# Performance work log

Hardware: AMD Instinct MI355X
Metric: run time of the kernel (lower is better)

Reference implementation:

```python
import jax, jax.numpy as jnp
import numpy as np

NUM_HEADS = 12
ROPE_THETA = 100.0

def _rotate_half(x):
    x1 = x[..., ::2]
    x2 = x[..., 1::2]
    return jnp.stack((-x2, x1), axis=-1).reshape(x.shape)

def _apply_rope(x, cos, sin):
    return x * cos + _rotate_half(x) * sin

def _rope_cos_sin(h, w, head_dim, theta):
    quarter = head_dim // 4  # head_dim=64 -> 16 freq bands
    inv_freq = 1.0 / theta ** (jnp.arange(quarter, dtype=jnp.float32) / max(quarter, 1))
    y = jnp.repeat(jnp.arange(h, dtype=jnp.float32), w)   # [h*w]
    xc = jnp.tile(jnp.arange(w, dtype=jnp.float32), h)    # [h*w]
    y_freqs = y[:, None] * inv_freq[None, :]               # [N, quarter]
    x_freqs = xc[:, None] * inv_freq[None, :]
    y_ang = jnp.repeat(y_freqs, 2, axis=-1)                # [N, half]
    x_ang = jnp.repeat(x_freqs, 2, axis=-1)
    ang = jnp.concatenate([y_ang, x_ang], axis=-1)         # [N, head_dim]
    return jnp.cos(ang)[None, None], jnp.sin(ang)[None, None]  # [1,1,N,hd]

def setup_inputs() -> dict:
    key = jax.random.key(0)
    ks = jax.random.split(key, 8)
    B, S, D = 8, 1025, 768
    s = 0.02
    return {
        "x": jax.random.normal(ks[0], (B, S, D), jnp.float32),
        "q_w": jax.random.normal(ks[1], (D, D), jnp.float32) * s,
        "q_b": jax.random.normal(ks[2], (D,), jnp.float32) * s,
        "k_w": jax.random.normal(ks[3], (D, D), jnp.float32) * s,
        "v_w": jax.random.normal(ks[4], (D, D), jnp.float32) * s,
        "v_b": jax.random.normal(ks[5], (D,), jnp.float32) * s,
        "o_w": jax.random.normal(ks[6], (D, D), jnp.float32) * s,
        "o_b": jax.random.normal(ks[7], (D,), jnp.float32) * s,
        "h": 32,
        "w": 32,
        "num_prefix_tokens": 1,
    }

def reference(x, q_w, q_b, k_w, v_w, v_b, o_w, o_b, h, w, num_prefix_tokens):
    B, S, D = x.shape
    H = NUM_HEADS
    hd = D // H
    scale = hd ** -0.5
    p = num_prefix_tokens

    def proj(W, b):
        y = jnp.einsum('bsd,ed->bse', x, W)
        if b is not None:
            y = y + b
        return y.reshape(B, S, H, hd).transpose(0, 2, 1, 3)  # [B,H,S,hd]

    q = proj(q_w, q_b)
    k = proj(k_w, None)
    v = proj(v_w, v_b)

    cos, sin = _rope_cos_sin(h, w, hd, ROPE_THETA)
    q = jnp.concatenate([q[:, :, :p], _apply_rope(q[:, :, p:], cos, sin)], axis=2)
    k = jnp.concatenate([k[:, :, :p], _apply_rope(k[:, :, p:], cos, sin)], axis=2)

    attn = jnp.einsum('bhqd,bhkd->bhqk', q * scale, k)
    attn = jax.nn.softmax(attn, axis=-1)
    out = jnp.einsum('bhqk,bhkd->bhqd', attn, v)
    out = out.transpose(0, 2, 1, 3).reshape(B, S, D)
    return jnp.einsum('bsd,ed->bse', out, o_w) + o_b
```

## Files before the change

kernel.cpp:

```cpp
#include <hip/hip_runtime.h>

typedef unsigned short u16;
typedef unsigned int   u32;
typedef __attribute__((ext_vector_type(4))) short s4;
typedef __attribute__((ext_vector_type(8))) short s8;
typedef __attribute__((ext_vector_type(4))) float f4;
typedef __attribute__((ext_vector_type(16))) float f16v;

#define NB   8
#define SEQ  1025
#define DIM  768
#define NH   12
#define HD   64
#define MV   8200
#define SQP  1040
#define SKP  1088
#define NG16 68
#define NQKV 2304
#define BHT  96
#define QSCALE 0.1803368801111204f

__device__ __forceinline__ u16 f2bf(float f) {
  u32 u = __builtin_bit_cast(u32, f);
  u += 0x7fffu + ((u >> 16) & 1u);
  return (u16)(u >> 16);
}
__device__ __forceinline__ float bf2f(u16 h) {
  return __builtin_bit_cast(float, ((u32)h) << 16);
}
__device__ __forceinline__ float exp2f_(float x) {
#if __has_builtin(__builtin_amdgcn_exp2f)
  return __builtin_amdgcn_exp2f(x);
#else
  return exp2f(x);
#endif
}
__device__ __forceinline__ u32 cvtpk(float a, float b) {
  u32 r;
  asm("v_cvt_pk_bf16_f32 %0, %1, %2" : "=v"(r) : "v"(a), "v"(b));
  return r;
}

typedef const __attribute__((address_space(1))) void cas1v;
typedef __attribute__((address_space(3))) void as3v;
__device__ __forceinline__ void gload16(const void* g, void* l) {
  __builtin_amdgcn_global_load_lds((cas1v*)g, (as3v*)l, 16, 0, 0);
}

#define MFMA16(a, b, c) __builtin_amdgcn_mfma_f32_16x16x32_bf16(a, b, c, 0, 0, 0)
#define MFMA32(a, b, c) __builtin_amdgcn_mfma_f32_32x32x16_bf16(a, b, c, 0, 0, 0)

__global__ void conv_x(const float* __restrict__ x, u16* __restrict__ xb) {
  int i = blockIdx.x * 256 + threadIdx.x;
  int e = i * 4;
  int row = e / DIM;
  s4 o;
  if (row < MV) {
    float4 v = *(const float4*)(x + e);
    o[0] = (short)f2bf(v.x); o[1] = (short)f2bf(v.y);
    o[2] = (short)f2bf(v.z); o[3] = (short)f2bf(v.w);
  } else {
    o = (s4){0, 0, 0, 0};
  }
  *(s4*)(xb + e) = o;
}

__global__ void conv_w(const float* __restrict__ qw, const float* __restrict__ kw,
                       const float* __restrict__ vw, const float* __restrict__ ow,
                       const float* __restrict__ qb, const float* __restrict__ vb,
                       u16* __restrict__ wqkv, u16* __restrict__ wo, float* __restrict__ biasq) {
  int i = blockIdx.x * 256 + threadIdx.x;
  wqkv[i]           = f2bf(qw[i]);
  wqkv[i + 589824]  = f2bf(kw[i]);
  wqkv[i + 1179648] = f2bf(vw[i]);
  wo[i]             = f2bf(ow[i]);
  if (i < NQKV) biasq[i] = (i < 768) ? qb[i] : (i < 1536 ? 0.f : vb[i - 1536]);
}

template <int MODE>
__global__ __launch_bounds__(256) void gemm_bt(const u16* __restrict__ A, const u16* __restrict__ Bm,
                                               float* __restrict__ Cf, const float* __restrict__ bias,
                                               u16* __restrict__ Ql, u16* __restrict__ Kl,
                                               u16* __restrict__ Vp,
                                               int N, int K, int Mvalid, int nnt) {
  __shared__ u16 As[2][128 * 32];
  __shared__ u16 Bs[2][128 * 32];
  int tid = threadIdx.x;
  int lane = tid & 63, wave = tid >> 6;
  int g = lane >> 4, c16 = lane & 15;
  int nwg = gridDim.x, orig = blockIdx.x;
  int qd = nwg >> 3, rm = nwg & 7, xcd = orig & 7;
  int wgid = (xcd < rm ? xcd * (qd + 1) : rm * (qd + 1) + (xcd - rm) * qd) + (orig >> 3);
  int m0 = (wgid / nnt) * 128, n0 = (wgid % nnt) * 128;
  int wm = wave >> 1, wn = wave & 1;
  f4 acc[4][4] = {};

  int ldrow = wave * 16 + (lane >> 2);
  int ldk = (lane & 3) * 8;
  const u16* Asrc = A + (size_t)(m0 + ldrow) * K + ldk;
  const u16* Bsrc = Bm + (size_t)(n0 + ldrow) * K + ldk;

  auto stage = [&](int buf, int k0) {
    u16* aw = &As[buf][wave * 512];
    u16* bw = &Bs[buf][wave * 512];
    gload16(Asrc + k0, aw);
    gload16(Asrc + 64 * K + k0, aw + 2048);
    gload16(Bsrc + k0, bw);
    gload16(Bsrc + 64 * K + k0, bw + 2048);
  };

  stage(0, 0);
  __syncthreads();
  int nk = K >> 5;
  for (int t = 0; t < nk; t++) {
    int buf = t & 1;
    if (t + 1 < nk) stage(buf ^ 1, (t + 1) << 5);
    s8 af[4], bf[4];
#pragma unroll
    for (int i = 0; i < 4; i++) {
      af[i] = *(const s8*)(&As[buf][(wm * 64 + i * 16 + c16) * 32 + g * 8]);
      bf[i] = *(const s8*)(&Bs[buf][(wn * 64 + i * 16 + c16) * 32 + g * 8]);
    }
    __builtin_amdgcn_s_setprio(1);
#pragma unroll
    for (int i = 0; i < 4; i++)
#pragma unroll
      for (int j = 0; j < 4; j++)
        acc[i][j] = MFMA16(af[i], bf[j], acc[i][j]);
    __builtin_amdgcn_s_setprio(0);
    __syncthreads();
  }

#pragma unroll
  for (int i = 0; i < 4; i++)
#pragma unroll
    for (int j = 0; j < 4; j++) {
      int n = n0 + wn * 64 + j * 16 + c16;
      float bv = bias[n];
#pragma unroll
      for (int r = 0; r < 4; r++) {
        int m = m0 + wm * 64 + i * 16 + g * 4 + r;
        if (m < Mvalid) {
          float v = acc[i][j][r] + bv;
          if (MODE == 1) {
            Cf[(size_t)m * N + n] = v;
          } else {
            int b = m / 1025, s = m - b * 1025;
            int nh6 = n >> 6, part = nh6 / 12, hq = nh6 - part * 12, d = n & 63;
            u16 o = f2bf(v);
            if (part == 0)      Ql[((size_t)((b * NH + hq) * SQP + s)) * HD + d] = o;
            else if (part == 1) Kl[((size_t)((b * NH + hq) * SKP + s)) * HD + d] = o;
            else {
              int g16 = s >> 4, rr = s & 15;
              int mp = (rr & 3) | (((rr >> 3) & 1) << 2) | (((rr >> 2) & 1) << 3);
              Vp[((size_t)((b * NH + hq) * NG16 + g16) * HD + d) * 16 + mp] = o;
            }
          }
        }
      }
    }
}

__global__ void rope_qk(u16* __restrict__ Ql, u16* __restrict__ Kl) {
  int t = blockIdx.x * 256 + threadIdx.x;
  int j = t & 31;
  int rem = t >> 5;
  int s = rem % SKP;
  int bh = rem / SKP;
  if (bh >= BHT) return;
  size_t qoff = ((size_t)(bh * SQP + s)) * HD + 2 * j;
  size_t koff = ((size_t)(bh * SKP + s)) * HD + 2 * j;
  if (s >= SEQ) {
    *(u32*)(Kl + koff) = 0;
    if (s < SQP) *(u32*)(Ql + qoff) = 0;
    return;
  }
  u32 qp = *(const u32*)(Ql + qoff);
  u32 kp = *(const u32*)(Kl + koff);
  float q0 = bf2f((u16)qp), q1 = bf2f((u16)(qp >> 16));
  float k0 = bf2f((u16)kp), k1 = bf2f((u16)(kp >> 16));
  float cs = 1.f, sn = 0.f;
  if (s > 0) {
    int tok = s - 1;
    int pos = (j < 16) ? (tok >> 5) : (tok & 31);
    int f = j & 15;
    float ang = (float)pos * __expf((float)f * -0.28782313662425572f);
    __sincosf(ang, &sn, &cs);
  }
  float q0r = q0 * cs - q1 * sn, q1r = q1 * cs + q0 * sn;
  float k0r = k0 * cs - k1 * sn, k1r = k1 * cs + k0 * sn;
  *(u32*)(Ql + qoff) = (u32)f2bf(q0r * QSCALE) | ((u32)f2bf(q1r * QSCALE) << 16);
  *(u32*)(Kl + koff) = (u32)f2bf(k0r) | ((u32)f2bf(k1r) << 16);
}

__global__ __launch_bounds__(256) void attn_k(const u16* __restrict__ Q, const u16* __restrict__ K,
                                              const u16* __restrict__ Vp, u16* __restrict__ Ao) {
  __shared__ u16 lds[2][2][64 * 64];
  int bh = blockIdx.x;
  int tid = threadIdx.x;
  int wave = tid >> 6, lane = tid & 63;
  int q32 = lane & 31, h = lane >> 5;
  int b = bh / NH, hh = bh % NH;
  int qb = blockIdx.y * 128 + wave * 32;
  if (qb > SEQ - 32) qb = SEQ - 32;
  const u16* Qb = Q + (size_t)bh * SQP * HD;
  const u16* Kb = K + (size_t)bh * SKP * HD;
  const u16* Vb = Vp + (size_t)bh * NG16 * 1024;

  s8 qf[4];
#pragma unroll
  for (int t = 0; t < 4; t++)
    qf[t] = *(const s8*)(Qb + (size_t)(qb + q32) * HD + 16 * t + 8 * h);

  f16v o0 = {}, o1 = {};
  float mrun = -3e38f, lrun = 0.f;
  int swz = (q32 & 7) << 4;

  auto stage = [&](int buf, int c) {
#pragma unroll
    for (int i = 0; i < 2; i++) {
      int sb = i * 4096 + tid * 16;
      int row = sb >> 7;
      int ch = (sb >> 4) & 7;
      int so = (ch ^ (row & 7)) * 8;
      u16* kd = &lds[buf][0][i * 2048 + wave * 512];
      u16* vd = &lds[buf][1][i * 2048 + wave * 512];
      gload16(Kb + (size_t)(c * 64 + row) * HD + so, kd);
      gload16(Vb + c * 4096 + i * 2048 + tid * 8, vd);
    }
  };

  stage(0, 0);
  __syncthreads();

  for (int c = 0; c < 17; c++) {
    int buf = c & 1;
    if (c < 16) stage(buf ^ 1, c + 1);
    const char* Ks = (const char*)&lds[buf][0][0];
    const char* Vs = (const char*)&lds[buf][1][0];

    f16v st0 = {}, st1 = {};
    __builtin_amdgcn_s_setprio(1);
#pragma unroll
    for (int t = 0; t < 4; t++) {
      int off = (32 * t + 16 * h) ^ swz;
      s8 a0 = *(const s8*)(Ks + q32 * 128 + off);
      s8 a1 = *(const s8*)(Ks + (32 + q32) * 128 + off);
      st0 = MFMA32(a0, qf[t], st0);
      st1 = MFMA32(a1, qf[t], st1);
    }
    __builtin_amdgcn_s_setprio(0);

    s8 vf0[4], vf1[4];
#pragma unroll
    for (int s = 0; s < 4; s++) {
      vf0[s] = *(const s8*)(Vs + 2048 * s + 32 * q32 + 16 * h);
      vf1[s] = *(const s8*)(Vs + 2048 * s + 1024 + 32 * q32 + 16 * h);
    }

    if (c == 16) {
      st0[0] = h ? -3e38f : st0[0];
#pragma unroll
      for (int r = 1; r < 16; r++) st0[r] = -3e38f;
#pragma unroll
      for (int r = 0; r < 16; r++) st1[r] = -3e38f;
    }

    float mx[8];
#pragma unroll
    for (int r = 0; r < 8; r++)
      mx[r] = fmaxf(fmaxf(st0[r], st0[r + 8]), fmaxf(st1[r], st1[r + 8]));
#pragma unroll
    for (int w = 4; w >= 1; w >>= 1)
#pragma unroll
      for (int r = 0; r < w; r++) mx[r] = fmaxf(mx[r], mx[r + w]);
    float pmax = fmaxf(mx[0], __shfl_xor(mx[0], 32));

    if (!__all(pmax <= mrun + 11.5f)) {
      float mnew = fmaxf(mrun, pmax);
      float cf = exp2f_(mrun - mnew);
      lrun *= cf;
      mrun = mnew;
#pragma unroll
      for (int r = 0; r < 16; r++) {
        float c2 = __shfl(cf, (r & 3) + 8 * (r >> 2) + 4 * h);
        o0[r] *= c2;
        o1[r] *= c2;
      }
    }

    float sm[8];
#pragma unroll
    for (int r = 0; r < 16; r++) {
      st0[r] = exp2f_(st0[r] - mrun);
      st1[r] = exp2f_(st1[r] - mrun);
    }
#pragma unroll
    for (int r = 0; r < 8; r++) sm[r] = (st0[r] + st0[r + 8]) + (st1[r] + st1[r + 8]);
#pragma unroll
    for (int w = 4; w >= 1; w >>= 1)
#pragma unroll
      for (int r = 0; r < w; r++) sm[r] += sm[r + w];
    lrun += sm[0] + __shfl_xor(sm[0], 32);

    __builtin_amdgcn_s_setprio(1);
#pragma unroll
    for (int s = 0; s < 4; s++) {
      union { s8 v; u32 w[4]; } pa;
#pragma unroll
      for (int i = 0; i < 4; i++) {
        float plo = (s < 2) ? st0[8 * (s & 1) + 2 * i]     : st1[8 * (s & 1) + 2 * i];
        float phi = (s < 2) ? st0[8 * (s & 1) + 2 * i + 1] : st1[8 * (s & 1) + 2 * i + 1];
        pa.w[i] = cvtpk(plo, phi);
      }
      o0 = MFMA32(pa.v, vf0[s], o0);
      o1 = MFMA32(pa.v, vf1[s], o1);
    }
    __builtin_amdgcn_s_setprio(0);
    __syncthreads();
  }

  float rl = 1.0f / lrun;
#pragma unroll
  for (int r = 0; r < 16; r++) {
    int cr = (r & 3) + 8 * (r >> 2) + 4 * h;
    float sc = __shfl(rl, cr);
    u16* dst = Ao + (size_t)(b * SEQ + qb + cr) * DIM + hh * HD;
    dst[q32]      = f2bf(o0[r] * sc);
    dst[32 + q32] = f2bf(o1[r] * sc);
  }
}

extern "C" void kernel_launch(void* const* d_in, const int* in_sizes, int n_in,
                              void* d_out, int out_size, void* d_ws, size_t ws_size,
                              hipStream_t stream) {
  const float* x  = (const float*)d_in[0];
  const float* qw = (const float*)d_in[1];
  const float* qb = (const float*)d_in[2];
  const float* kw = (const float*)d_in[3];
  const float* vw = (const float*)d_in[4];
  const float* vb = (const float*)d_in[5];
  const float* ow = (const float*)d_in[6];
  const float* ob = (const float*)d_in[7];
  float* out = (float*)d_out;

  char* ws = (char*)d_ws;
  u16*   xb   = (u16*)(ws);
  u16*   wqkv = (u16*)(ws + 12779520);
  u16*   wo   = (u16*)(ws + 16318464);
  float* bq   = (float*)(ws + 17498112);
  u16*   Ql   = (u16*)(ws + 17507328);
  u16*   Kl   = (u16*)(ws + 30286848);
  u16*   Vp   = (u16*)(ws + 43656192);
  u16*   Ao   = xb;

  conv_x<<<6240, 256, 0, stream>>>(x, xb);
  conv_w<<<2304, 256, 0, stream>>>(qw, kw, vw, ow, qb, vb, wqkv, wo, bq);
  hipMemsetAsync(Vp, 0, 13369344, stream);
  gemm_bt<2><<<1170, 256, 0, stream>>>(xb, wqkv, nullptr, bq, Ql, Kl, Vp, NQKV, DIM, MV, 18);
  rope_qk<<<13056, 256, 0, stream>>>(Ql, Kl);
  attn_k<<<dim3(96, 9), 256, 0, stream>>>(Ql, Kl, Vp, Ao);
  gemm_bt<1><<<390, 256, 0, stream>>>(Ao, wo, out, ob, nullptr, nullptr, nullptr, DIM, DIM, MV, 6);
}
```

Before: 171.1 us.

## Fuse RoPE and Q scaling into QKV GEMM epilogue with LDS-staged stores

Removes the separate RoPE kernel and the V memset. RoPE and Q scaling are now applied in the QKV GEMM epilogue, using a cos/sin table that the weight-conversion kernel precomputes. The input is repacked into a per-batch padded layout (1040 rows), so GEMM tiles line up with sequence padding. The epilogue stages each tile in LDS and writes Q/K/V with 16-byte vector stores, and the LDS tiles use an XOR swizzle to cut bank conflicts. In exchange, K/V padding rows beyond those the GEMM writes are no longer explicitly zeroed, and the epilogue gains a shuffle, a table lookup and an extra barrier.

```diff
diff --git a/kernel.cpp b/kernel.cpp
--- a/kernel.cpp
+++ b/kernel.cpp
@@ -12,6 +12,8 @@
 #define DIM  768
 #define NH   12
 #define HD   64
+#define BPAD 1040
+#define MPAD 8320
 #define MV   8200
 #define SQP  1040
 #define SKP  1088
@@ -53,10 +55,11 @@
 __global__ void conv_x(const float* __restrict__ x, u16* __restrict__ xb) {
   int i = blockIdx.x * 256 + threadIdx.x;
   int e = i * 4;
-  int row = e / DIM;
+  int row = e / DIM, col = e - row * DIM;
+  int b = row / BPAD, s = row - b * BPAD;
   s4 o;
-  if (row < MV) {
-    float4 v = *(const float4*)(x + e);
+  if (s < SEQ) {
+    float4 v = *(const float4*)(x + ((size_t)(b * SEQ + s)) * DIM + col);
     o[0] = (short)f2bf(v.x); o[1] = (short)f2bf(v.y);
     o[2] = (short)f2bf(v.z); o[3] = (short)f2bf(v.w);
   } else {
@@ -68,23 +71,36 @@
 __global__ void conv_w(const float* __restrict__ qw, const float* __restrict__ kw,
                        const float* __restrict__ vw, const float* __restrict__ ow,
                        const float* __restrict__ qb, const float* __restrict__ vb,
-                       u16* __restrict__ wqkv, u16* __restrict__ wo, float* __restrict__ biasq) {
+                       u16* __restrict__ wqkv, u16* __restrict__ wo, float* __restrict__ biasq,
+                       float2* __restrict__ rt) {
   int i = blockIdx.x * 256 + threadIdx.x;
   wqkv[i]           = f2bf(qw[i]);
   wqkv[i + 589824]  = f2bf(kw[i]);
   wqkv[i + 1179648] = f2bf(vw[i]);
   wo[i]             = f2bf(ow[i]);
   if (i < NQKV) biasq[i] = (i < 768) ? qb[i] : (i < 1536 ? 0.f : vb[i - 1536]);
+  if (i < SEQ * 32) {
+    int s = i >> 5, jj = i & 31;
+    float cs = 1.f, sn = 0.f;
+    if (s > 0) {
+      int tok = s - 1;
+      int pos = (jj < 16) ? (tok >> 5) : (tok & 31);
+      int f = jj & 15;
+      float ang = (float)pos * __expf((float)f * -0.28782313662425572f);
+      __sincosf(ang, &sn, &cs);
+    }
+    rt[i] = make_float2(cs, sn);
+  }
 }
 
 template <int MODE>
 __global__ __launch_bounds__(256) void gemm_bt(const u16* __restrict__ A, const u16* __restrict__ Bm,
                                                float* __restrict__ Cf, const float* __restrict__ bias,
                                                u16* __restrict__ Ql, u16* __restrict__ Kl,
-                                               u16* __restrict__ Vp,
+                                               u16* __restrict__ Vp, const float2* __restrict__ rt,
                                                int N, int K, int Mvalid, int nnt) {
-  __shared__ u16 As[2][128 * 32];
-  __shared__ u16 Bs[2][128 * 32];
+  __shared__ u16 smem[16640];
+  u16 (*ct)[130] = (u16(*)[130])smem;
   int tid = threadIdx.x;
   int lane = tid & 63, wave = tid >> 6;
   int g = lane >> 4, c16 = lane & 15;
@@ -96,13 +112,13 @@
   f4 acc[4][4] = {};
 
   int ldrow = wave * 16 + (lane >> 2);
-  int ldk = (lane & 3) * 8;
+  int ldk = ((lane & 3) ^ ((ldrow >> 1) & 3)) * 8;
   const u16* Asrc = A + (size_t)(m0 + ldrow) * K + ldk;
   const u16* Bsrc = Bm + (size_t)(n0 + ldrow) * K + ldk;
 
   auto stage = [&](int buf, int k0) {
-    u16* aw = &As[buf][wave * 512];
-    u16* bw = &Bs[buf][wave * 512];
+    u16* aw = smem + buf * 4096 + wave * 512;
+    u16* bw = smem + 8192 + buf * 4096 + wave * 512;
     gload16(Asrc + k0, aw);
     gload16(Asrc + 64 * K + k0, aw + 2048);
     gload16(Bsrc + k0, bw);
@@ -112,14 +128,15 @@
   stage(0, 0);
   __syncthreads();
   int nk = K >> 5;
+  int kx = (g ^ ((c16 >> 1) & 3)) * 8;
   for (int t = 0; t < nk; t++) {
     int buf = t & 1;
     if (t + 1 < nk) stage(buf ^ 1, (t + 1) << 5);
     s8 af[4], bf[4];
 #pragma unroll
     for (int i = 0; i < 4; i++) {
-      af[i] = *(const s8*)(&As[buf][(wm * 64 + i * 16 + c16) * 32 + g * 8]);
-      bf[i] = *(const s8*)(&Bs[buf][(wn * 64 + i * 16 + c16) * 32 + g * 8]);
+      af[i] = *(const s8*)(smem + buf * 4096 + (wm * 64 + i * 16 + c16) * 32 + kx);
+      bf[i] = *(const s8*)(smem + 8192 + buf * 4096 + (wn * 64 + i * 16 + c16) * 32 + kx);
     }
     __builtin_amdgcn_s_setprio(1);
 #pragma unroll
@@ -131,66 +148,85 @@
     __syncthreads();
   }
 
-#pragma unroll
-  for (int i = 0; i < 4; i++)
+  if (MODE == 1) {
+#pragma unroll
+    for (int i = 0; i < 4; i++)
+#pragma unroll
+      for (int j = 0; j < 4; j++) {
+        int n = n0 + wn * 64 + j * 16 + c16;
+        float bv = bias[n];
+#pragma unroll
+        for (int r = 0; r < 4; r++) {
+          int m = m0 + wm * 64 + i * 16 + g * 4 + r;
+          if (m < Mvalid) Cf[(size_t)m * N + n] = acc[i][j][r] + bv;
+        }
+      }
+  } else {
+    int part = (n0 >= 1536) ? 2 : (n0 >= 768 ? 1 : 0);
+    float qs = (part == 0) ? QSCALE : 1.0f;
 #pragma unroll
     for (int j = 0; j < 4; j++) {
-      int n = n0 + wn * 64 + j * 16 + c16;
-      float bv = bias[n];
-#pragma unroll
-      for (int r = 0; r < 4; r++) {
-        int m = m0 + wm * 64 + i * 16 + g * 4 + r;
-        if (m < Mvalid) {
+      int col = wn * 64 + j * 16 + c16;
+      float bv = bias[n0 + col];
+      int jj = (col & 63) >> 1;
+      int odd = col & 1;
+#pragma unroll
+      for (int i = 0; i < 4; i++) {
+        int rowb = wm * 64 + i * 16 + g * 4;
+#pragma unroll
+        for (int r = 0; r < 4; r++) {
           float v = acc[i][j][r] + bv;
-          if (MODE == 1) {
-            Cf[(size_t)m * N + n] = v;
+          u16 o;
+          if (part < 2) {
+            float vp = __shfl_xor(v, 1);
+            int m = m0 + rowb + r;
+            int s = m % BPAD;
+            float2 t = rt[(s < SEQ ? s : SEQ - 1) * 32 + jj];
+            float rv = odd ? (v * t.x + vp * t.y) : (v * t.x - vp * t.y);
+            o = f2bf(rv * qs);
           } else {
-            int b = m / 1025, s = m - b * 1025;
-            int nh6 = n >> 6, part = nh6 / 12, hq = nh6 - part * 12, d = n & 63;
-            u16 o = f2bf(v);
-            if (part == 0)      Ql[((size_t)((b * NH + hq) * SQP + s)) * HD + d] = o;
-            else if (part == 1) Kl[((size_t)((b * NH + hq) * SKP + s)) * HD + d] = o;
-            else {
-              int g16 = s >> 4, rr = s & 15;
-              int mp = (rr & 3) | (((rr >> 3) & 1) << 2) | (((rr >> 2) & 1) << 3);
-              Vp[((size_t)((b * NH + hq) * NG16 + g16) * HD + d) * 16 + mp] = o;
-            }
+            o = f2bf(v);
           }
+          ct[rowb + r][col] = o;
         }
       }
     }
-}
-
-__global__ void rope_qk(u16* __restrict__ Ql, u16* __restrict__ Kl) {
-  int t = blockIdx.x * 256 + threadIdx.x;
-  int j = t & 31;
-  int rem = t >> 5;
-  int s = rem % SKP;
-  int bh = rem / SKP;
-  if (bh >= BHT) return;
-  size_t qoff = ((size_t)(bh * SQP + s)) * HD + 2 * j;
-  size_t koff = ((size_t)(bh * SKP + s)) * HD + 2 * j;
-  if (s >= SEQ) {
-    *(u32*)(Kl + koff) = 0;
-    if (s < SQP) *(u32*)(Ql + qoff) = 0;
-    return;
-  }
-  u32 qp = *(const u32*)(Ql + qoff);
-  u32 kp = *(const u32*)(Kl + koff);
-  float q0 = bf2f((u16)qp), q1 = bf2f((u16)(qp >> 16));
-  float k0 = bf2f((u16)kp), k1 = bf2f((u16)(kp >> 16));
-  float cs = 1.f, sn = 0.f;
-  if (s > 0) {
-    int tok = s - 1;
-    int pos = (j < 16) ? (tok >> 5) : (tok & 31);
-    int f = j & 15;
-    float ang = (float)pos * __expf((float)f * -0.28782313662425572f);
-    __sincosf(ang, &sn, &cs);
-  }
-  float q0r = q0 * cs - q1 * sn, q1r = q1 * cs + q0 * sn;
-  float k0r = k0 * cs - k1 * sn, k1r = k1 * cs + k0 * sn;
-  *(u32*)(Ql + qoff) = (u32)f2bf(q0r * QSCALE) | ((u32)f2bf(q1r * QSCALE) << 16);
-  *(u32*)(Kl + koff) = (u32)f2bf(k0r) | ((u32)f2bf(k1r) << 16);
+    __syncthreads();
+    if (part < 2) {
+      u16* dstB = (part == 0) ? Ql : Kl;
+      int stride = (part == 0) ? SQP : SKP;
+#pragma unroll
+      for (int p = 0; p < 8; p++) {
+        int task = p * 256 + tid;
+        int row = task >> 4, cg = (task & 15) * 8;
+        int m = m0 + row, b = m / BPAD, s = m - b * BPAD;
+        int n = n0 + cg;
+        int hq = (n >> 6) - part * NH;
+        s8 v = *(const s8*)&ct[row][cg];
+        *(s8*)(dstB + ((size_t)((b * NH + hq) * stride + s)) * HD + (n & 63)) = v;
+      }
+    } else {
+#pragma unroll
+      for (int p = 0; p < 4; p++) {
+        int task = p * 256 + tid;
+        int col = task & 127, rg = task >> 7;
+        int mb = m0 + rg * 16, b = mb / BPAD, sb = mb - b * BPAD;
+        int g16 = sb >> 4;
+        int n = n0 + col;
+        int hq = (n >> 6) - 2 * NH;
+        s8 o0, o1;
+#pragma unroll
+        for (int k = 0; k < 16; k++) {
+          int mp = (k & 3) | (((k >> 3) & 1) << 2) | (((k >> 2) & 1) << 3);
+          u16 val = ct[rg * 16 + k][col];
+          if (mp < 8) o0[mp] = (short)val; else o1[mp - 8] = (short)val;
+        }
+        u16* dst = Vp + ((size_t)((b * NH + hq) * NG16 + g16) * HD + (n & 63)) * 16;
+        *(s8*)dst = o0;
+        *(s8*)(dst + 8) = o1;
+      }
+    }
+  }
 }
 
 __global__ __launch_bounds__(256) void attn_k(const u16* __restrict__ Q, const u16* __restrict__ K,
@@ -345,20 +381,19 @@
   float* out = (float*)d_out;
 
   char* ws = (char*)d_ws;
-  u16*   xb   = (u16*)(ws);
-  u16*   wqkv = (u16*)(ws + 12779520);
-  u16*   wo   = (u16*)(ws + 16318464);
-  float* bq   = (float*)(ws + 17498112);
-  u16*   Ql   = (u16*)(ws + 17507328);
-  u16*   Kl   = (u16*)(ws + 30286848);
-  u16*   Vp   = (u16*)(ws + 43656192);
-  u16*   Ao   = xb;
+  u16*    xb   = (u16*)(ws);
+  u16*    wqkv = (u16*)(ws + 12779520);
+  u16*    wo   = (u16*)(ws + 16318464);
+  float*  bq   = (float*)(ws + 17498112);
+  float2* rt   = (float2*)(ws + 17507328);
+  u16*    Ql   = (u16*)(ws + 17769728);
+  u16*    Kl   = (u16*)(ws + 30549248);
+  u16*    Vp   = (u16*)(ws + 43918592);
+  u16*    Ao   = xb;
 
   conv_x<<<6240, 256, 0, stream>>>(x, xb);
-  conv_w<<<2304, 256, 0, stream>>>(qw, kw, vw, ow, qb, vb, wqkv, wo, bq);
-  hipMemsetAsync(Vp, 0, 13369344, stream);
-  gemm_bt<2><<<1170, 256, 0, stream>>>(xb, wqkv, nullptr, bq, Ql, Kl, Vp, NQKV, DIM, MV, 18);
-  rope_qk<<<13056, 256, 0, stream>>>(Ql, Kl);
+  conv_w<<<2304, 256, 0, stream>>>(qw, kw, vw, ow, qb, vb, wqkv, wo, bq, rt);
+  gemm_bt<2><<<1170, 256, 0, stream>>>(xb, wqkv, nullptr, bq, Ql, Kl, Vp, rt, NQKV, DIM, MPAD, 18);
   attn_k<<<dim3(96, 9), 256, 0, stream>>>(Ql, Kl, Vp, Ao);
-  gemm_bt<1><<<390, 256, 0, stream>>>(Ao, wo, out, ob, nullptr, nullptr, nullptr, DIM, DIM, MV, 6);
-}
+  gemm_bt<1><<<390, 256, 0, stream>>>(Ao, wo, out, ob, nullptr, nullptr, nullptr, rt, DIM, DIM, MV, 6);
+}
```

Result: faster. 155.6 us (-9.0%).
